# Kernel optimization log

Measured on AMD Instinct MI355X. Metric: run time of the kernel, lower is better.

## Reference

```python
import jax, jax.numpy as jnp
import numpy as np

H, W = 240, 320          # dim from init_kwargs
S = 48                   # hardcoded segment count
SIDX = 4                 # startIdx
EIDX = S - 10            # S - endBias
KSIZE = 5
KVALS = [0.03125, 0.03125, 0.01562, 0.03125, 0.03125,
         0.03125, 0.04406, 0.03125, 0.04406, 0.03125,
         0.0425, 0.0625, 0.14502, 0.0625, 0.0425,
         0.03125, 0.04406, 0.03125, 0.04406, 0.03125,
         0.03125, 0.03125, 0.01562, 0.03125, 0.03125]


def setup_inputs() -> dict:
    key = jax.random.key(0)
    B, N = 32, 393216
    kx, ky, kr = jax.random.split(key, 3)
    x = jax.random.randint(kx, (B, N), 0, W, dtype=jnp.int32)
    y = jax.random.randint(ky, (B, N), 0, H, dtype=jnp.int32)
    rest = jax.random.randint(kr, (B, N, 3), 0, 2, dtype=jnp.int32)  # t,p,b unused
    events = jnp.concatenate([x[..., None], y[..., None], rest], axis=-1)
    blur_kernel = jnp.array(KVALS, dtype=jnp.float32).reshape(KSIZE, KSIZE)
    return {"events": events, "blur_kernel": blur_kernel}


def _blur(h, kernel):
    # h: [B,1,S,D]; depthwise conv with the same 5x5 kernel per batch (groups=B in torch)
    k = kernel.reshape(1, 1, KSIZE, KSIZE)
    return jax.lax.conv_general_dilated(
        h, k, (1, 1), [(2, 2), (2, 2)],
        dimension_numbers=('NCHW', 'OIHW', 'NCHW'))


def _mean_curve(coord, seg, D, segLen, kernel):
    # coord: [B,usable] int32 in [0,D); seg: [usable] segment id per event
    B = coord.shape[0]
    flat = (jnp.arange(B, dtype=jnp.int32)[:, None] * (S * D)
            + seg[None, :] * D + coord)
    hist = jnp.zeros((B * S * D,), jnp.int32).at[flat.reshape(-1)].add(1)
    hist = hist.reshape(B, 1, S, D).astype(jnp.float32)
    hist = _blur(hist, kernel)[:, 0]                                  # [B,S,D]
    mean = jnp.einsum('bsd,d->bs', hist,
                      jnp.arange(D, dtype=jnp.float32)) / jnp.float32(segLen)
    start = mean[:, SIDX:SIDX + 1]
    dis_to_center = (D // 2) - start
    aligned = jnp.round(mean - start - dis_to_center).astype(jnp.int32)
    return mean, aligned


def _outlier_first(mean):
    # outlier1d (MAD-based) on each 10-wide window starting at si, flag for element 0
    idx = jnp.arange(SIDX + 1, EIDX)[:, None] + jnp.arange(10)[None, :]  # [n,10]
    win = mean[:, idx]                                                    # [B,n,10]
    med = jnp.median(win, axis=-1, keepdims=True)
    diff = jnp.abs(win - med)
    mad = jnp.median(diff, axis=-1)
    mz = 0.6745 * diff[..., 0] / mad
    return mz > 3.0                                                       # [B,n]


def _normalize(v):
    v = v.astype(jnp.float32)
    clamp = jnp.mean(v) + 3.0 * jnp.std(v, ddof=1)   # torch std is unbiased
    return jnp.clip(v, 0.0, clamp) / clamp


def _process_one(idx_rows, out_flags):
    # idx_rows: [S, segLen] flat pixel indices; out_flags: [EIDX-SIDX-1] bool
    HW = H * W
    segLen = idx_rows.shape[1]
    ones = jnp.ones((segLen,), jnp.int32)
    container = jnp.zeros((HW,), jnp.int32).at[idx_rows[SIDX]].add(ones)
    v0 = jnp.zeros((HW,), bool).at[idx_rows[SIDX]].set(True)
    v1 = jnp.ones((HW,), bool)
    conf = jnp.zeros((HW,), jnp.int32)

    def step(carry, inp):
        container, v0, v1, conf, stopped = carry
        row, is_out = inp
        active = jnp.logical_and(~stopped, ~is_out)   # 'continue' on outlier
        vnew_raw = jnp.zeros((HW,), bool).at[row].set(True)
        conf = jnp.where(active,
                         conf + (vnew_raw & v0 & v1).astype(jnp.int32), conf)
        vnew = vnew_raw | v0
        new_info = jnp.logical_xor(vnew, v0).sum().astype(jnp.float32)
        ratio = new_info / vnew.sum().astype(jnp.float32)
        small = ratio < 0.01                           # 'break' condition
        do_upd = active & (~small)
        container = jnp.where(do_upd, container.at[row].add(ones), container)
        v1 = jnp.where(do_upd, v0, v1)
        v0 = jnp.where(do_upd, vnew, v0)
        stopped = stopped | (active & small)
        return (container, v0, v1, conf, stopped), None

    carry0 = (container, v0, v1, conf, jnp.array(False))
    (container, v0, v1, conf, _), _ = jax.lax.scan(
        step, carry0, (idx_rows[SIDX + 1:EIDX], out_flags))
    return jnp.stack([_normalize(container), _normalize(conf)]).reshape(2, H, W)


def reference(events, blur_kernel):
    B, N, _ = events.shape
    segLen = N // S
    usable = segLen * S
    x = events[:, :usable, 0]
    y = events[:, :usable, 1]
    seg = (jnp.arange(usable, dtype=jnp.int32) // segLen).astype(jnp.int32)
    meanX, alignedX = _mean_curve(x, seg, W, segLen, blur_kernel)
    meanY, alignedY = _mean_curve(y, seg, H, segLen, blur_kernel)
    outl = _outlier_first(meanX) | _outlier_first(meanY)      # [B, 33]
    xx = jnp.clip(x - jnp.take(alignedX, seg, axis=1), 0, W - 1)
    yy = jnp.clip(y - jnp.take(alignedY, seg, axis=1), 0, H - 1)
    idx = (xx + W * yy).reshape(B, S, segLen)
    return jax.vmap(_process_one)(idx, outl)                  # [B,2,H,W]
```

## Files before the change

kernel.cpp:

```cpp
#include <hip/hip_runtime.h>
#include <math.h>

#define BB      32
#define NN      393216
#define SS      48
#define SEGLEN  8192
#define WW      320
#define HH      240
#define HWSZ    76800
#define NWORDS  2400
#define NSEG    34
#define NWIN    33
#define NWPT    10
#define NG      8
#define HW4     19200
#define NPC     75
#define NPF     10

__global__ __launch_bounds__(256) void k_hist(const int* __restrict__ ev,
                                              int* __restrict__ histX,
                                              int* __restrict__ histY,
                                              unsigned* __restrict__ packed,
                                              int use_packed) {
    int bs = blockIdx.x;
    int b = bs / SS, s = bs % SS;
    __shared__ int hx[WW];
    __shared__ int hy[HH];
    for (int i = threadIdx.x; i < WW; i += 256) hx[i] = 0;
    for (int i = threadIdx.x; i < HH; i += 256) hy[i] = 0;
    __syncthreads();
    size_t ebase = ((size_t)b * NN + (size_t)s * SEGLEN);
    size_t ibase = ebase * 5;
    const int4* ev4 = (const int4*)(ev + ibase);
    int t = threadIdx.x;
    int lane = t & 63;
    #pragma unroll 2
    for (int it = 0; it < 40; ++it) {
        int q = it * 256 + t;
        int4 v = ev4[q];
        int m = q % 5;
        int xv, yv;
        switch (m) {
            case 0:  xv = v.x; yv = v.y; break;
            case 1:  xv = v.y; yv = v.z; break;
            case 2:  xv = v.z; yv = v.w; break;
            case 3:  xv = v.w; yv = 0;   break;
            default: xv = -1;  yv = v.x; break;
        }
        int nb = __shfl_down(v.x, 1);
        if (m == 3)
            yv = (lane == 63) ? ev[ibase + 4 * (size_t)(q + 1)] : nb;
        if (m != 3) atomicAdd(&hy[yv], 1);
        if (m != 4) {
            atomicAdd(&hx[xv], 1);
            if (use_packed) {
                int e = (4 * q + m) / 5;
                packed[ebase + e] = (unsigned)xv | ((unsigned)yv << 16);
            }
        }
    }
    __syncthreads();
    for (int i = threadIdx.x; i < WW; i += 256) histX[(size_t)bs * WW + i] = hx[i];
    for (int i = threadIdx.x; i < HH; i += 256) histY[(size_t)bs * HH + i] = hy[i];
}

__device__ double conv_mean_partial(const int* __restrict__ histB, const float* kk,
                                    int s, int D, int t) {
    double acc = 0.0;
    for (int d = t; d < D; d += 256) {
        double c = 0.0;
        #pragma unroll
        for (int i = 0; i < 5; ++i) {
            int ss = s - 2 + i;
            if (ss < 0 || ss >= SS) continue;
            const int* row = histB + (size_t)ss * D;
            #pragma unroll
            for (int j = 0; j < 5; ++j) {
                int dd = d - 2 + j;
                if ((unsigned)dd < (unsigned)D)
                    c += (double)kk[i * 5 + j] * (double)row[dd];
            }
        }
        acc += c * (double)d;
    }
    return acc;
}

__global__ __launch_bounds__(256) void k_mean(const int* __restrict__ histX,
                                              const int* __restrict__ histY,
                                              const float* __restrict__ kern,
                                              float* __restrict__ meanX,
                                              float* __restrict__ meanY) {
    int bs = blockIdx.x;
    int b = bs / SS, s = bs % SS;
    int t = threadIdx.x;
    __shared__ float kk[25];
    __shared__ double red[256];
    if (t < 25) kk[t] = kern[t];
    __syncthreads();

    double accX = conv_mean_partial(histX + (size_t)b * SS * WW, kk, s, WW, t);
    red[t] = accX;
    __syncthreads();
    for (int off = 128; off > 0; off >>= 1) {
        if (t < off) red[t] += red[t + off];
        __syncthreads();
    }
    if (t == 0) meanX[bs] = (float)(red[0] / (double)SEGLEN);
    __syncthreads();

    double accY = conv_mean_partial(histY + (size_t)b * SS * HH, kk, s, HH, t);
    red[t] = accY;
    __syncthreads();
    for (int off = 128; off > 0; off >>= 1) {
        if (t < off) red[t] += red[t + off];
        __syncthreads();
    }
    if (t == 0) meanY[bs] = (float)(red[0] / (double)SEGLEN);
}

__device__ bool outlier_win(const float* w) {
    float a[10], srt[10];
    #pragma unroll
    for (int i = 0; i < 10; ++i) { a[i] = w[i]; srt[i] = w[i]; }
    for (int i = 1; i < 10; ++i) {
        float v = srt[i]; int j = i - 1;
        while (j >= 0 && srt[j] > v) { srt[j + 1] = srt[j]; --j; }
        srt[j + 1] = v;
    }
    float med = 0.5f * (srt[4] + srt[5]);
    float d[10];
    #pragma unroll
    for (int i = 0; i < 10; ++i) d[i] = fabsf(a[i] - med);
    float d0 = d[0];
    for (int i = 1; i < 10; ++i) {
        float v = d[i]; int j = i - 1;
        while (j >= 0 && d[j] > v) { d[j + 1] = d[j]; --j; }
        d[j + 1] = v;
    }
    float mad = 0.5f * (d[4] + d[5]);
    float mz = 0.6745f * d0 / mad;
    return mz > 3.0f;
}

__global__ __launch_bounds__(64) void k_align_outl(const float* __restrict__ meanX,
                                                   const float* __restrict__ meanY,
                                                   int* __restrict__ alignedX,
                                                   int* __restrict__ alignedY,
                                                   int* __restrict__ outl) {
    int b = blockIdx.x, t = threadIdx.x;
    __shared__ float mX[SS], mY[SS];
    if (t < SS) { mX[t] = meanX[b * SS + t]; mY[t] = meanY[b * SS + t]; }
    __syncthreads();
    if (t < SS) {
        float sX = mX[4];
        float dX = (float)(WW / 2) - sX;
        alignedX[b * SS + t] = (int)rintf((mX[t] - sX) - dX);
        float sY = mY[4];
        float dY = (float)(HH / 2) - sY;
        alignedY[b * SS + t] = (int)rintf((mY[t] - sY) - dY);
    }
    if (t < NWIN) {
        int i = 5 + t;
        bool f = outlier_win(&mX[i]) || outlier_win(&mY[i]);
        outl[b * NWIN + t] = f ? 1 : 0;
    }
}

__global__ __launch_bounds__(256) void k_bitmap(const int* __restrict__ ev,
                                                const unsigned* __restrict__ packed,
                                                int use_packed,
                                                const int* __restrict__ alignedX,
                                                const int* __restrict__ alignedY,
                                                unsigned* __restrict__ bitmaps) {
    int b = blockIdx.x / NSEG;
    int si = blockIdx.x % NSEG;
    int s = 4 + si;
    __shared__ unsigned bm[NWORDS];
    for (int w = threadIdx.x; w < NWORDS; w += 256) bm[w] = 0u;
    __syncthreads();
    int ax = alignedX[b * SS + s];
    int ay = alignedY[b * SS + s];
    size_t ebase = ((size_t)b * NN + (size_t)s * SEGLEN);
    for (int i = threadIdx.x; i < SEGLEN; i += 256) {
        int x, y;
        if (use_packed) {
            unsigned p = packed[ebase + i];
            x = (int)(p & 0xFFFFu);
            y = (int)(p >> 16);
        } else {
            x = ev[(ebase + i) * 5 + 0];
            y = ev[(ebase + i) * 5 + 1];
        }
        int xx = min(max(x - ax, 0), WW - 1);
        int yy = min(max(y - ay, 0), HH - 1);
        int p = xx + WW * yy;
        atomicOr(&bm[p >> 5], 1u << (p & 31));
    }
    __syncthreads();
    unsigned* dst = bitmaps + ((size_t)b * NSEG + si) * NWORDS;
    for (int w = threadIdx.x; w < NWORDS; w += 256) dst[w] = bm[w];
}

__global__ __launch_bounds__(256) void k_decide(const unsigned* __restrict__ bitmaps,
                                                const int* __restrict__ outl,
                                                int* __restrict__ code,
                                                int* __restrict__ updFlag) {
    int b = blockIdx.x, t = threadIdx.x;
    const unsigned* base = bitmaps + (size_t)b * NSEG * NWORDS;
    unsigned v0r[NWPT];
    #pragma unroll
    for (int k = 0; k < NWPT; ++k) {
        int w = t + k * 256;
        v0r[k] = (w < NWORDS) ? base[w] : 0u;
    }
    __shared__ int redN[4], redT[4];
    __shared__ int dec;
    if (t < SS) updFlag[b * SS + t] = 0;
    bool stopped = false;
    for (int s = 5; s <= 37; ++s) {
        int c = 0;
        if (!stopped && !outl[b * NWIN + (s - 5)]) {
            const unsigned* Vs = base + (size_t)(s - 4) * NWORDS;
            int ni = 0, tot = 0;
            #pragma unroll
            for (int k = 0; k < NWPT; ++k) {
                int w = t + k * 256;
                if (w < NWORDS) {
                    unsigned raw = Vs[w];
                    ni += __popc(raw & ~v0r[k]);
                    tot += __popc(raw | v0r[k]);
                }
            }
            #pragma unroll
            for (int off = 32; off > 0; off >>= 1) {
                ni += __shfl_down(ni, off);
                tot += __shfl_down(tot, off);
            }
            if ((t & 63) == 0) { redN[t >> 6] = ni; redT[t >> 6] = tot; }
            __syncthreads();
            if (t == 0) {
                int N = redN[0] + redN[1] + redN[2] + redN[3];
                int T = redT[0] + redT[1] + redT[2] + redT[3];
                float ratio = (float)N / (float)T;
                dec = (ratio < 0.01f) ? 1 : 2;
            }
            __syncthreads();
            if (dec == 2) {
                #pragma unroll
                for (int k = 0; k < NWPT; ++k) {
                    int w = t + k * 256;
                    if (w < NWORDS) v0r[k] |= Vs[w];
                }
                c = 2;
            } else {
                stopped = true;
                c = 1;
            }
        }
        if (t == 0) {
            code[b * NWIN + (s - 5)] = c;
            if (c == 2) updFlag[b * SS + s] = 1;
        }
    }
}

__global__ __launch_bounds__(256) void k_conf(const unsigned* __restrict__ bitmaps,
                                              const int* __restrict__ code,
                                              int* __restrict__ conf,
                                              long long* __restrict__ partF) {
    int b = blockIdx.y;
    int t = threadIdx.x;
    int w = blockIdx.x * 256 + t;
    __shared__ int sc[NWIN];
    if (t < NWIN) sc[t] = code[b * NWIN + t];
    __syncthreads();
    long long s1 = 0, s2 = 0;
    if (w < NWORDS) {
        const unsigned* base = bitmaps + (size_t)b * NSEG * NWORDS;
        unsigned v0 = base[w];
        unsigned vv = v0;
        unsigned c0 = 0, c1 = 0, c2 = 0, c3 = 0, c4 = 0, c5 = 0;
        for (int s = 5; s <= 37; ++s) {
            int cd = sc[s - 5];
            if (cd == 0) continue;
            unsigned raw = base[(size_t)(s - 4) * NWORDS + w];
            unsigned carry = raw & vv, nc;
            nc = c0 & carry; c0 ^= carry; carry = nc;
            nc = c1 & carry; c1 ^= carry; carry = nc;
            nc = c2 & carry; c2 ^= carry; carry = nc;
            nc = c3 & carry; c3 ^= carry; carry = nc;
            nc = c4 & carry; c4 ^= carry; carry = nc;
            c5 ^= carry;
            if (cd == 2) { vv = v0; v0 |= raw; }
        }
        int* dst = conf + (size_t)b * HWSZ + (size_t)w * 32;
        #pragma unroll
        for (int j = 0; j < 32; ++j) {
            int v = (int)((c0 >> j) & 1u) | ((int)((c1 >> j) & 1u) << 1)
                  | ((int)((c2 >> j) & 1u) << 2) | ((int)((c3 >> j) & 1u) << 3)
                  | ((int)((c4 >> j) & 1u) << 4) | ((int)((c5 >> j) & 1u) << 5);
            dst[j] = v;
            s1 += v;
            s2 += (long long)v * v;
        }
    }
    #pragma unroll
    for (int off = 32; off > 0; off >>= 1) {
        s1 += __shfl_down(s1, off);
        s2 += __shfl_down(s2, off);
    }
    __shared__ long long r1[4], r2[4];
    if ((t & 63) == 0) { r1[t >> 6] = s1; r2[t >> 6] = s2; }
    __syncthreads();
    if (t == 0) {
        long long S1 = r1[0] + r1[1] + r1[2] + r1[3];
        long long S2 = r2[0] + r2[1] + r2[2] + r2[3];
        partF[((size_t)b * NPF + blockIdx.x) * 2 + 0] = S1;
        partF[((size_t)b * NPF + blockIdx.x) * 2 + 1] = S2;
    }
}

__global__ __launch_bounds__(256) void k_hcount(const int* __restrict__ ev,
                                                const unsigned* __restrict__ packed,
                                                int use_packed,
                                                const int* __restrict__ alignedX,
                                                const int* __restrict__ alignedY,
                                                const int* __restrict__ updFlag,
                                                unsigned* __restrict__ planes) {
    int g = blockIdx.x, b = blockIdx.y;
    __shared__ unsigned hist[HW4];
    for (int i = threadIdx.x; i < HW4; i += 256) hist[i] = 0u;
    __syncthreads();
    for (int si = g; si < NSEG; si += NG) {
        int s = 4 + si;
        if (si != 0 && updFlag[b * SS + s] == 0) continue;
        int ax = alignedX[b * SS + s];
        int ay = alignedY[b * SS + s];
        size_t ebase = ((size_t)b * NN + (size_t)s * SEGLEN);
        for (int i = threadIdx.x; i < SEGLEN; i += 256) {
            int x, y;
            if (use_packed) {
                unsigned p = packed[ebase + i];
                x = (int)(p & 0xFFFFu);
                y = (int)(p >> 16);
            } else {
                x = ev[(ebase + i) * 5 + 0];
                y = ev[(ebase + i) * 5 + 1];
            }
            int xx = min(max(x - ax, 0), WW - 1);
            int yy = min(max(y - ay, 0), HH - 1);
            int p = xx + WW * yy;
            atomicAdd(&hist[p >> 2], 1u << (8 * (p & 3)));
        }
    }
    __syncthreads();
    unsigned* dst = planes + ((size_t)b * NG + g) * HW4;
    for (int i = threadIdx.x; i < HW4; i += 256) dst[i] = hist[i];
}

__global__ __launch_bounds__(256) void k_merge(const unsigned* __restrict__ planes,
                                               int* __restrict__ container,
                                               long long* __restrict__ partC) {
    int b = blockIdx.y;
    int t = threadIdx.x;
    int w = blockIdx.x * 256 + t;
    int c0 = 0, c1 = 0, c2 = 0, c3 = 0;
    #pragma unroll
    for (int g = 0; g < NG; ++g) {
        unsigned v = planes[((size_t)b * NG + g) * HW4 + w];
        c0 += (int)(v & 255u);
        c1 += (int)((v >> 8) & 255u);
        c2 += (int)((v >> 16) & 255u);
        c3 += (int)(v >> 24);
    }
    int4 o; o.x = c0; o.y = c1; o.z = c2; o.w = c3;
    ((int4*)(container + (size_t)b * HWSZ))[w] = o;
    long long s1 = c0 + c1 + c2 + c3;
    long long s2 = (long long)c0 * c0 + (long long)c1 * c1
                 + (long long)c2 * c2 + (long long)c3 * c3;
    #pragma unroll
    for (int off = 32; off > 0; off >>= 1) {
        s1 += __shfl_down(s1, off);
        s2 += __shfl_down(s2, off);
    }
    __shared__ long long r1[4], r2[4];
    if ((t & 63) == 0) { r1[t >> 6] = s1; r2[t >> 6] = s2; }
    __syncthreads();
    if (t == 0) {
        long long S1 = r1[0] + r1[1] + r1[2] + r1[3];
        long long S2 = r2[0] + r2[1] + r2[2] + r2[3];
        partC[((size_t)b * NPC + blockIdx.x) * 2 + 0] = S1;
        partC[((size_t)b * NPC + blockIdx.x) * 2 + 1] = S2;
    }
}

__global__ __launch_bounds__(64) void k_clamp(const long long* __restrict__ partC,
                                              const long long* __restrict__ partF,
                                              float* __restrict__ clamps) {
    int id = blockIdx.x;
    int b = id >> 1, arr = id & 1;
    const long long* p = arr ? (partF + (size_t)b * NPF * 2)
                             : (partC + (size_t)b * NPC * 2);
    int n = arr ? NPF : NPC;
    int t = threadIdx.x;
    long long s1 = 0, s2 = 0;
    for (int i = t; i < n; i += 64) { s1 += p[i * 2]; s2 += p[i * 2 + 1]; }
    #pragma unroll
    for (int off = 32; off > 0; off >>= 1) {
        s1 += __shfl_down(s1, off);
        s2 += __shfl_down(s2, off);
    }
    if (t == 0) {
        double nn = (double)HWSZ;
        double sum = (double)s1, sumsq = (double)s2;
        double meanv = sum / nn;
        double var = (sumsq - sum * sum / nn) / (nn - 1.0);
        if (var < 0.0) var = 0.0;
        clamps[id] = (float)(meanv + 3.0 * sqrt(var));
    }
}

__global__ __launch_bounds__(256) void k_container(const int* __restrict__ ev,
                                                   const unsigned* __restrict__ packed,
                                                   int use_packed,
                                                   const int* __restrict__ alignedX,
                                                   const int* __restrict__ alignedY,
                                                   const int* __restrict__ updFlag,
                                                   int* __restrict__ container) {
    int b = blockIdx.x / NSEG;
    int si = blockIdx.x % NSEG;
    int s = 4 + si;
    if (si != 0 && updFlag[b * SS + s] == 0) return;
    int ax = alignedX[b * SS + s];
    int ay = alignedY[b * SS + s];
    int* cb = container + (size_t)b * HWSZ;
    size_t ebase = ((size_t)b * NN + (size_t)s * SEGLEN);
    for (int i = threadIdx.x; i < SEGLEN; i += 256) {
        int x, y;
        if (use_packed) {
            unsigned p = packed[ebase + i];
            x = (int)(p & 0xFFFFu);
            y = (int)(p >> 16);
        } else {
            x = ev[(ebase + i) * 5 + 0];
            y = ev[(ebase + i) * 5 + 1];
        }
        int xx = min(max(x - ax, 0), WW - 1);
        int yy = min(max(y - ay, 0), HH - 1);
        atomicAdd(&cb[xx + WW * yy], 1);
    }
}

__global__ __launch_bounds__(256) void k_stats(const int* __restrict__ container,
                                               const int* __restrict__ conf,
                                               float* __restrict__ clamps) {
    int id = blockIdx.x;
    int b = id >> 1, arr = id & 1;
    const int* src = (arr ? conf : container) + (size_t)b * HWSZ;
    int t = threadIdx.x;
    long long s1 = 0, s2 = 0;
    for (int i = t; i < HWSZ; i += 256) {
        long long v = src[i];
        s1 += v;
        s2 += v * v;
    }
    __shared__ long long r1[256], r2[256];
    r1[t] = s1; r2[t] = s2;
    __syncthreads();
    for (int off = 128; off > 0; off >>= 1) {
        if (t < off) { r1[t] += r1[t + off]; r2[t] += r2[t + off]; }
        __syncthreads();
    }
    if (t == 0) {
        double n = (double)HWSZ;
        double sum = (double)r1[0], sumsq = (double)r2[0];
        double meanv = sum / n;
        double var = (sumsq - sum * sum / n) / (n - 1.0);
        if (var < 0.0) var = 0.0;
        clamps[id] = (float)(meanv + 3.0 * sqrt(var));
    }
}

__global__ __launch_bounds__(256) void k_out(const int* __restrict__ container,
                                             const int* __restrict__ conf,
                                             const float* __restrict__ clamps,
                                             float* __restrict__ out) {
    size_t idx = (size_t)blockIdx.x * 256 + threadIdx.x;
    int b = (int)(idx / (2 * HWSZ));
    int r = (int)(idx % (2 * HWSZ));
    int arr = r / HWSZ;
    int p = r % HWSZ;
    int v = (arr ? conf : container)[(size_t)b * HWSZ + p];
    float c = clamps[b * 2 + arr];
    out[idx] = fminf((float)v, c) / c;
}

extern "C" void kernel_launch(void* const* d_in, const int* in_sizes, int n_in,
                              void* d_out, int out_size, void* d_ws, size_t ws_size,
                              hipStream_t stream) {
    const int* ev = (const int*)d_in[0];
    const float* kern = (const float*)d_in[1];
    float* out = (float*)d_out;

    char* ws = (char*)d_ws;
    size_t o = 0;
    auto alloc = [&](size_t bytes) {
        size_t r = o;
        o += (bytes + 255) & ~(size_t)255;
        return r;
    };
    int*      histX    = (int*)      (ws + alloc((size_t)BB * SS * WW * 4));
    int*      histY    = (int*)      (ws + alloc((size_t)BB * SS * HH * 4));
    float*    meanX    = (float*)    (ws + alloc((size_t)BB * SS * 4));
    float*    meanY    = (float*)    (ws + alloc((size_t)BB * SS * 4));
    int*      alignedX = (int*)      (ws + alloc((size_t)BB * SS * 4));
    int*      alignedY = (int*)      (ws + alloc((size_t)BB * SS * 4));
    int*      outl     = (int*)      (ws + alloc((size_t)BB * NWIN * 4));
    unsigned* bitmaps  = (unsigned*) (ws + alloc((size_t)BB * NSEG * NWORDS * 4));
    int*      updFlag  = (int*)      (ws + alloc((size_t)BB * SS * 4));
    int*      code     = (int*)      (ws + alloc((size_t)BB * NWIN * 4));
    float*    clamps   = (float*)    (ws + alloc((size_t)BB * 2 * 4));
    long long* partC   = (long long*)(ws + alloc((size_t)BB * NPC * 2 * 8));
    long long* partF   = (long long*)(ws + alloc((size_t)BB * NPF * 2 * 8));
    int*      container= (int*)      (ws + alloc((size_t)BB * HWSZ * 4));
    int*      conf     = (int*)      (ws + alloc((size_t)BB * HWSZ * 4));
    size_t planes_off = alloc((size_t)BB * NG * HW4 * 4);
    int use_planes = (o <= ws_size) ? 1 : 0;
    unsigned* planes = use_planes ? (unsigned*)(ws + planes_off) : (unsigned*)ws;
    size_t packed_off = alloc((size_t)BB * NN * 4);
    int use_packed = (o <= ws_size) ? 1 : 0;
    unsigned* packed = use_packed ? (unsigned*)(ws + packed_off) : (unsigned*)ws;

    k_hist      <<<BB * SS,   256, 0, stream>>>(ev, histX, histY, packed, use_packed);
    k_mean      <<<BB * SS,   256, 0, stream>>>(histX, histY, kern, meanX, meanY);
    k_align_outl<<<BB,         64, 0, stream>>>(meanX, meanY, alignedX, alignedY, outl);
    k_bitmap    <<<BB * NSEG, 256, 0, stream>>>(ev, packed, use_packed, alignedX, alignedY, bitmaps);
    k_decide    <<<BB,        256, 0, stream>>>(bitmaps, outl, code, updFlag);
    {
        dim3 grid(NPF, BB);
        k_conf  <<<grid,      256, 0, stream>>>(bitmaps, code, conf, partF);
    }
    if (use_planes) {
        dim3 g1(NG, BB);
        k_hcount<<<g1,        256, 0, stream>>>(ev, packed, use_packed, alignedX, alignedY, updFlag, planes);
        dim3 g2(NPC, BB);
        k_merge <<<g2,        256, 0, stream>>>(planes, container, partC);
        k_clamp <<<BB * 2,     64, 0, stream>>>(partC, partF, clamps);
    } else {
        hipMemsetAsync(container, 0, (size_t)BB * HWSZ * 4, stream);
        k_container<<<BB * NSEG, 256, 0, stream>>>(ev, packed, use_packed, alignedX, alignedY, updFlag, container);
        k_stats <<<BB * 2,    256, 0, stream>>>(container, conf, clamps);
    }
    k_out       <<<(BB * 2 * HWSZ) / 256, 256, 0, stream>>>(container, conf, clamps, out);
}
```

Baseline: 555.3 us.

## Use single-wave k_decide, double NG histogram groups, vectorize k_out

k_decide now runs as one 64-lane wavefront per batch with 38 words per lane held in registers. This removes the shared-memory reductions and the two block barriers in each of the 33 sequential steps, and the loaded row is reused for the OR update instead of being read again. NG goes from 8 to 16, which doubles the per-batch parallelism of the hcount/planes path. k_out now processes four elements per thread with int4/float4 accesses. The wider register arrays can raise register pressure, and with only 32 single-wave blocks k_decide has little latency hiding.

```diff
diff --git a/kernel.cpp b/kernel.cpp
--- a/kernel.cpp
+++ b/kernel.cpp
@@ -11,11 +11,11 @@
 #define NWORDS  2400
 #define NSEG    34
 #define NWIN    33
-#define NWPT    10
-#define NG      8
+#define NG      16
 #define HW4     19200
 #define NPC     75
 #define NPF     10
+#define DW      38
 
 __global__ __launch_bounds__(256) void k_hist(const int* __restrict__ ev,
                                               int* __restrict__ histX,
@@ -202,63 +202,53 @@
     for (int w = threadIdx.x; w < NWORDS; w += 256) dst[w] = bm[w];
 }
 
-__global__ __launch_bounds__(256) void k_decide(const unsigned* __restrict__ bitmaps,
-                                                const int* __restrict__ outl,
-                                                int* __restrict__ code,
-                                                int* __restrict__ updFlag) {
-    int b = blockIdx.x, t = threadIdx.x;
+__global__ __launch_bounds__(64) void k_decide(const unsigned* __restrict__ bitmaps,
+                                               const int* __restrict__ outl,
+                                               int* __restrict__ code,
+                                               int* __restrict__ updFlag) {
+    int b = blockIdx.x;
+    int lane = threadIdx.x;
     const unsigned* base = bitmaps + (size_t)b * NSEG * NWORDS;
-    unsigned v0r[NWPT];
-    #pragma unroll
-    for (int k = 0; k < NWPT; ++k) {
-        int w = t + k * 256;
+    unsigned v0r[DW];
+    #pragma unroll
+    for (int k = 0; k < DW; ++k) {
+        int w = lane + (k << 6);
         v0r[k] = (w < NWORDS) ? base[w] : 0u;
     }
-    __shared__ int redN[4], redT[4];
-    __shared__ int dec;
-    if (t < SS) updFlag[b * SS + t] = 0;
+    if (lane < SS) updFlag[b * SS + lane] = 0;
     bool stopped = false;
     for (int s = 5; s <= 37; ++s) {
         int c = 0;
         if (!stopped && !outl[b * NWIN + (s - 5)]) {
             const unsigned* Vs = base + (size_t)(s - 4) * NWORDS;
+            unsigned raw[DW];
+            #pragma unroll
+            for (int k = 0; k < DW; ++k) {
+                int w = lane + (k << 6);
+                raw[k] = (w < NWORDS) ? Vs[w] : 0u;
+            }
             int ni = 0, tot = 0;
             #pragma unroll
-            for (int k = 0; k < NWPT; ++k) {
-                int w = t + k * 256;
-                if (w < NWORDS) {
-                    unsigned raw = Vs[w];
-                    ni += __popc(raw & ~v0r[k]);
-                    tot += __popc(raw | v0r[k]);
-                }
+            for (int k = 0; k < DW; ++k) {
+                ni  += __popc(raw[k] & ~v0r[k]);
+                tot += __popc(raw[k] | v0r[k]);
             }
             #pragma unroll
-            for (int off = 32; off > 0; off >>= 1) {
-                ni += __shfl_down(ni, off);
-                tot += __shfl_down(tot, off);
-            }
-            if ((t & 63) == 0) { redN[t >> 6] = ni; redT[t >> 6] = tot; }
-            __syncthreads();
-            if (t == 0) {
-                int N = redN[0] + redN[1] + redN[2] + redN[3];
-                int T = redT[0] + redT[1] + redT[2] + redT[3];
-                float ratio = (float)N / (float)T;
-                dec = (ratio < 0.01f) ? 1 : 2;
-            }
-            __syncthreads();
-            if (dec == 2) {
-                #pragma unroll
-                for (int k = 0; k < NWPT; ++k) {
-                    int w = t + k * 256;
-                    if (w < NWORDS) v0r[k] |= Vs[w];
-                }
-                c = 2;
-            } else {
+            for (int off = 1; off < 64; off <<= 1) {
+                ni  += __shfl_xor(ni, off);
+                tot += __shfl_xor(tot, off);
+            }
+            float ratio = (float)ni / (float)tot;
+            if (ratio < 0.01f) {
                 stopped = true;
                 c = 1;
-            }
-        }
-        if (t == 0) {
+            } else {
+                c = 2;
+                #pragma unroll
+                for (int k = 0; k < DW; ++k) v0r[k] |= raw[k];
+            }
+        }
+        if (lane == 0) {
             code[b * NWIN + (s - 5)] = c;
             if (c == 2) updFlag[b * SS + s] = 1;
         }
@@ -486,14 +476,20 @@
                                              const int* __restrict__ conf,
                                              const float* __restrict__ clamps,
                                              float* __restrict__ out) {
-    size_t idx = (size_t)blockIdx.x * 256 + threadIdx.x;
-    int b = (int)(idx / (2 * HWSZ));
-    int r = (int)(idx % (2 * HWSZ));
-    int arr = r / HWSZ;
-    int p = r % HWSZ;
-    int v = (arr ? conf : container)[(size_t)b * HWSZ + p];
+    size_t idx4 = (size_t)blockIdx.x * 256 + threadIdx.x;
+    int b   = (int)(idx4 / (2 * (HWSZ / 4)));
+    int r   = (int)(idx4 % (2 * (HWSZ / 4)));
+    int arr = r / (HWSZ / 4);
+    int p4  = r % (HWSZ / 4);
+    const int4* src = (const int4*)((arr ? conf : container) + (size_t)b * HWSZ);
+    int4 v = src[p4];
     float c = clamps[b * 2 + arr];
-    out[idx] = fminf((float)v, c) / c;
+    float4 o;
+    o.x = fminf((float)v.x, c) / c;
+    o.y = fminf((float)v.y, c) / c;
+    o.z = fminf((float)v.z, c) / c;
+    o.w = fminf((float)v.w, c) / c;
+    ((float4*)out)[idx4] = o;
 }
 
 extern "C" void kernel_launch(void* const* d_in, const int* in_sizes, int n_in,
@@ -536,7 +532,7 @@
     k_mean      <<<BB * SS,   256, 0, stream>>>(histX, histY, kern, meanX, meanY);
     k_align_outl<<<BB,         64, 0, stream>>>(meanX, meanY, alignedX, alignedY, outl);
     k_bitmap    <<<BB * NSEG, 256, 0, stream>>>(ev, packed, use_packed, alignedX, alignedY, bitmaps);
-    k_decide    <<<BB,        256, 0, stream>>>(bitmaps, outl, code, updFlag);
+    k_decide    <<<BB,         64, 0, stream>>>(bitmaps, outl, code, updFlag);
     {
         dim3 grid(NPF, BB);
         k_conf  <<<grid,      256, 0, stream>>>(bitmaps, code, conf, partF);
@@ -552,5 +548,5 @@
         k_container<<<BB * NSEG, 256, 0, stream>>>(ev, packed, use_packed, alignedX, alignedY, updFlag, container);
         k_stats <<<BB * 2,    256, 0, stream>>>(container, conf, clamps);
     }
-    k_out       <<<(BB * 2 * HWSZ) / 256, 256, 0, stream>>>(container, conf, clamps, out);
-}
+    k_out       <<<(BB * 2 * HWSZ) / 1024, 256, 0, stream>>>(container, conf, clamps, out);
+}
```

Measured after the change: 514.0 us. -7.5%, faster.
